# Kernel tuning notes

Measured on AMD Instinct MI355X. Metric: run time of the kernel, lower is better.

Reference implementation:

```python
import jax, jax.numpy as jnp
import numpy as np

B, L, D = 4096, 200, 32
NUM_USERS, NUM_GOODS, NUM_CATS = 49023, 143534, 4815
ATT_H1, ATT_H2 = 80, 40
MLP_H1, MLP_H2 = 200, 80
NEG_INF = jnp.float32(-2**32 + 1)


def prelu(x, a):
    return jnp.where(x >= 0, x, a * x)


def setup_inputs() -> dict:
    key = jax.random.key(0)
    ks = jax.random.split(key, 24)
    g = lambda k, shape, fan_in: jax.random.normal(k, shape, jnp.float32) * (1.0 / np.sqrt(fan_in))
    return {
        "uid": jax.random.randint(ks[0], (B,), 0, NUM_USERS, jnp.int32),
        "gid": jax.random.randint(ks[1], (B,), 0, NUM_GOODS, jnp.int32),
        "cid": jax.random.randint(ks[2], (B,), 0, NUM_CATS, jnp.int32),
        "gid_his": jax.random.randint(ks[3], (B, L), 0, NUM_GOODS, jnp.int32),
        "cid_his": jax.random.randint(ks[4], (B, L), 0, NUM_CATS, jnp.int32),
        "masks": jax.random.randint(ks[5], (B, L), 0, 2, jnp.int32),
        # frozen embedding tables
        "user_emb": jax.random.normal(ks[6], (NUM_USERS, D), jnp.float32),
        "good_emb": jax.random.normal(ks[7], (NUM_GOODS, D), jnp.float32),
        "cat_emb": jax.random.normal(ks[8], (NUM_CATS, D), jnp.float32),
        # attention MLP: 8D -> 80 -> 40 -> 1, sigmoid activations
        "att_w1": g(ks[9], (ATT_H1, 8 * D), 8 * D), "att_b1": jnp.zeros((ATT_H1,), jnp.float32),
        "att_w2": g(ks[10], (ATT_H2, ATT_H1), ATT_H1), "att_b2": jnp.zeros((ATT_H2,), jnp.float32),
        "att_w3": g(ks[11], (1, ATT_H2), ATT_H2), "att_b3": jnp.zeros((1,), jnp.float32),
        # final MLP: 9D -> 200 -> 80 -> 2, PReLU activations
        "mlp_w1": g(ks[12], (MLP_H1, 9 * D), 9 * D), "mlp_b1": jnp.zeros((MLP_H1,), jnp.float32),
        "mlp_w2": g(ks[13], (MLP_H2, MLP_H1), MLP_H1), "mlp_b2": jnp.zeros((MLP_H2,), jnp.float32),
        "mlp_w3": g(ks[14], (2, MLP_H2), MLP_H2), "mlp_b3": jnp.zeros((2,), jnp.float32),
        "a1": jnp.full((MLP_H1,), 0.25, jnp.float32),
        "a2": jnp.full((MLP_H2,), 0.25, jnp.float32),
    }


def reference(uid, gid, cid, gid_his, cid_his, masks,
              user_emb, good_emb, cat_emb,
              att_w1, att_b1, att_w2, att_b2, att_w3, att_b3,
              mlp_w1, mlp_b1, mlp_w2, mlp_b2, mlp_w3, mlp_b3, a1, a2):
    user = user_emb[uid]                                              # (B, D)
    query = jnp.concatenate([good_emb[gid], cat_emb[cid]], -1)        # (B, 2D)
    beh = jnp.concatenate([good_emb[gid_his], cat_emb[cid_his]], -1)  # (B, L, 2D)

    # attention: concat(query, behavior, diff, product) -> tiny MLP -> masked softmax pool
    q = jnp.broadcast_to(query[:, None, :], beh.shape)                # (B, L, 2D)
    s = jnp.concatenate([q, beh, q - beh, q * beh], -1)               # (B, L, 8D)
    s = jax.nn.sigmoid(jnp.einsum('blk,hk->blh', s, att_w1) + att_b1)
    s = jax.nn.sigmoid(jnp.einsum('blh,gh->blg', s, att_w2) + att_b2)
    s = jnp.einsum('blg,og->blo', s, att_w3) + att_b3                 # (B, L, 1)
    s = jnp.where(masks[..., None].astype(bool), s, NEG_INF)
    w = jax.nn.softmax(s, axis=1)
    att = jnp.sum(w * beh, axis=1)                                    # (B, 2D)

    ubs = beh.sum(axis=1)                                             # (B, 2D)
    x = jnp.concatenate([user, query, ubs, ubs * query, att], -1)     # (B, 9D)
    x = prelu(x @ mlp_w1.T + mlp_b1, a1)
    x = prelu(x @ mlp_w2.T + mlp_b2, a2)
    return x @ mlp_w3.T + mlp_b3                                      # (B, 2)
```

## Files before the change

kernel.cpp:

```cpp
#include <hip/hip_runtime.h>
#include <math.h>

typedef unsigned short u16;
typedef unsigned int u32;
typedef __attribute__((ext_vector_type(8))) short short8;
typedef __attribute__((ext_vector_type(8))) float f32x8;
typedef __attribute__((ext_vector_type(4))) float f32x4;
typedef __attribute__((ext_vector_type(2))) unsigned int uint2v;

#define NEG_BIG   (-4294967296.0f)
#define NEG_INF_F (-__builtin_inff())

#define WS_S    0
#define WS_W1T  5120
#define WS_W2T  62720
#define WS_W3T  78720
#define WS_W3P  78880
#define WS_WF1F 78928
#define WS_WF2F 84048
#define WS_XF   86352

__device__ __forceinline__ u32 f2bf2(float lo, float hi) {
    u32 r;
    asm("v_cvt_pk_bf16_f32 %0, %1, %2" : "=v"(r) : "v"(lo), "v"(hi));
    return r;
}
__device__ __forceinline__ u16 f2bf(float f) {
    u32 r;
    asm("v_cvt_pk_bf16_f32 %0, %1, %1" : "=v"(r) : "v"(f));
    return (u16)r;
}
__device__ __forceinline__ float bf2f(u16 h) {
    union { u32 u; float f; } v; v.u = ((u32)h) << 16;
    return v.f;
}
__device__ __forceinline__ float fsigmoid(float x) {
    float e, r;
    float t = x * -1.44269504088896f;
    asm("v_exp_f32 %0, %1" : "=v"(e) : "v"(t));
    float d = 1.0f + e;
    asm("v_rcp_f32 %0, %1" : "=v"(r) : "v"(d));
    return r;
}
__device__ __forceinline__ short8 mulqf(short8 a, f32x8 qf) {
    union { u32 w[4]; short8 s; } r;
    #pragma unroll
    for (int j = 0; j < 4; ++j) {
        float p0 = bf2f((u16)a[2*j])   * qf[2*j];
        float p1 = bf2f((u16)a[2*j+1]) * qf[2*j+1];
        r.w[j] = f2bf2(p0, p1);
    }
    return r.s;
}
__device__ __forceinline__ f32x4 mfma16(short8 a, short8 b, f32x4 c) {
    return __builtin_amdgcn_mfma_f32_16x16x32_bf16(a, b, c, 0, 0, 0);
}

__global__ __launch_bounds__(256) void prep_kernel(
    const float* __restrict__ att_w1,
    const float* __restrict__ att_w2,
    const float* __restrict__ att_w3,
    const float* __restrict__ mlp_w1,
    const float* __restrict__ mlp_w2,
    const float* __restrict__ mlp_w3,
    float* __restrict__ ws)
{
    int idx = blockIdx.x * 256 + threadIdx.x;
    if (idx < 5120) {
        int h = idx >> 6, j = idx & 63;
        ws[WS_S + idx] = att_w1[h*256 + j] + att_w1[h*256 + 128 + j];
    } else if (idx < 62720) {
        int r = idx - 5120;
        int k = r / 200, t = r - k*200;
        ws[WS_W1T + r] = mlp_w1[t*288 + k];
    } else if (idx < 78720) {
        int r = idx - 62720;
        int k = r / 80, g = r - k*80;
        ws[WS_W2T + r] = mlp_w2[g*200 + k];
    } else if (idx < 78880) {
        int r = idx - 78720;
        int k = r >> 1, o = r & 1;
        ws[WS_W3T + r] = mlp_w3[o*80 + k];
    } else if (idx < 78928) {
        int g = idx - 78880;
        ws[WS_W3P + g] = (g < 40) ? att_w3[g] : 0.0f;
    } else if (idx < 89168) {
        int e  = idx - 78928;
        int nt = e >> 11;
        int ks = (e >> 9) & 3;
        int ln = (e >> 3) & 63;
        int j  = e & 7;
        int n = nt*16 + (ln & 15);
        int k = ks*32 + (ln >> 4)*8 + j;
        float val = (k < 64)
            ? (att_w1[n*256 + 64 + k] - att_w1[n*256 + 128 + k])
            : att_w1[n*256 + 192 + (k - 64)];
        ((u16*)(ws + WS_WF1F))[e] = f2bf(val);
    } else if (idx < 93776) {
        int e  = idx - 89168;
        int nt = e / 1536;
        int ks = (e / 512) % 3;
        int ln = (e >> 3) & 63;
        int j  = e & 7;
        int n = nt*16 + (ln & 15);
        int k = ks*32 + (ln >> 4)*8 + j;
        float val = (n < 40 && k < 80) ? att_w2[n*80 + k] : 0.0f;
        ((u16*)(ws + WS_WF2F))[e] = f2bf(val);
    }
}

__global__ __launch_bounds__(256) void din_kernel(
    const int* __restrict__ uid, const int* __restrict__ gid, const int* __restrict__ cid,
    const int* __restrict__ gid_his, const int* __restrict__ cid_his, const int* __restrict__ masks,
    const float* __restrict__ user_emb, const float* __restrict__ good_emb, const float* __restrict__ cat_emb,
    const float* __restrict__ att_b1, const float* __restrict__ att_b2, const float* __restrict__ att_b3,
    const float* __restrict__ ws, float* __restrict__ Xg)
{
    __shared__ u16 Xc[200*64];
    __shared__ u16 scr[4*1664];
    __shared__ float q_sh[64];
    __shared__ float c0_sh[80];
    __shared__ float sp_sh[256];
    __shared__ float scal_sh[2];

    float* redA  = (float*)scr;
    float* redU  = redA + 512;

    const int b    = blockIdx.x;
    const int tid  = threadIdx.x;
    const int lane = tid & 63;
    const int wv   = tid >> 6;
    const int lrow = lane & 15;
    const int lgrp = lane >> 4;

    const int* gh = gid_his + b*200;
    const int* ch = cid_his + b*200;

    short8 wf1r[20];
    short8 wf2r[9];
    float  w3v[10];
    {
        const short8* WF1 = (const short8*)(ws + WS_WF1F);
        const short8* WF2 = (const short8*)(ws + WS_WF2F);
        #pragma unroll
        for (int i = 0; i < 20; ++i) wf1r[i] = WF1[i*64 + lane];
        #pragma unroll
        for (int i = 0; i < 9; ++i)  wf2r[i] = WF2[i*64 + lane];
        #pragma unroll
        for (int i = 0; i < 10; ++i) w3v[i] = ws[WS_W3P + lgrp + 4*i];
    }

    #pragma unroll
    for (int it = 0; it < 12; ++it) {
        int idx = it*256 + tid;
        int l = idx >> 4, c = idx & 15;
        const float* src = (c < 8)
            ? (good_emb + (size_t)gh[l]*32 + (c & 7)*4)
            : (cat_emb  + (size_t)ch[l]*32 + (c & 7)*4);
        float4 v = *(const float4*)src;
        uint2v pk;
        pk[0] = f2bf2(v.x, v.y);
        pk[1] = f2bf2(v.z, v.w);
        int byteoff = l*128 + ((((c >> 1) ^ (l & 7)) << 4)) + ((c & 1) << 3);
        *((uint2v*)((char*)Xc + byteoff)) = pk;
    }
    if (tid < 128) {
        int idx = 3072 + tid;
        int l = idx >> 4, c = idx & 15;
        const float* src = (c < 8)
            ? (good_emb + (size_t)gh[l]*32 + (c & 7)*4)
            : (cat_emb  + (size_t)ch[l]*32 + (c & 7)*4);
        float4 v = *(const float4*)src;
        uint2v pk;
        pk[0] = f2bf2(v.x, v.y);
        pk[1] = f2bf2(v.z, v.w);
        int byteoff = l*128 + ((((c >> 1) ^ (l & 7)) << 4)) + ((c & 1) << 3);
        *((uint2v*)((char*)Xc + byteoff)) = pk;
    }
    if (tid < 64) {
        q_sh[tid] = (tid < 32) ? good_emb[(size_t)gid[b]*32 + tid]
                               : cat_emb[(size_t)cid[b]*32 + (tid - 32)];
    }
    if (tid >= 200 && tid < 256) sp_sh[tid] = NEG_INF_F;
    __syncthreads();

    if (tid < 80) {
        const float4* Sw = (const float4*)(ws + WS_S + tid*64);
        const float4* q4 = (const float4*)q_sh;
        float u0 = 0.f, u1 = 0.f;
        #pragma unroll
        for (int j = 0; j < 16; j += 2) {
            float4 w0 = Sw[j],   qv0 = q4[j];
            float4 w1 = Sw[j+1], qv1 = q4[j+1];
            u0 += w0.x*qv0.x + w0.y*qv0.y + w0.z*qv0.z + w0.w*qv0.w;
            u1 += w1.x*qv1.x + w1.y*qv1.y + w1.z*qv1.z + w1.w*qv1.w;
        }
        c0_sh[tid] = att_b1[tid] + u0 + u1;
    }
    __syncthreads();

    f32x8 qf0, qf1;
    #pragma unroll
    for (int j = 0; j < 8; ++j) {
        qf0[j] = q_sh[lgrp*8 + j];
        qf1[j] = q_sh[32 + lgrp*8 + j];
    }
    float c0v[5];
    #pragma unroll
    for (int nt = 0; nt < 5; ++nt) c0v[nt] = c0_sh[nt*16 + lrow];
    float b2v[3];
    #pragma unroll
    for (int nt = 0; nt < 3; ++nt) {
        int col = nt*16 + lrow;
        b2v[nt] = (col < 40) ? att_b2[col] : 0.0f;
    }
    const float bias3 = att_b3[0];

    u16*   scr_w = scr + wv*1664;
    float* scr_f = (float*)scr_w;

    {
        uint2v z; z[0] = 0u; z[1] = 0u;
        *((uint2v*)(scr_w + lrow*104 + 80 + lgrp*4)) = z;
    }

    for (int t = wv; t < 13; t += 4) {
        const int m0 = (t == 12) ? 184 : (t << 4);
        const int m  = m0 + lrow;

        short8 A0, A1;
        {
            int sl0 = (0 + lgrp) ^ (m & 7);
            int sl1 = (4 + lgrp) ^ (m & 7);
            A0 = *(const short8*)((const char*)Xc + m*128 + (sl0 << 4));
            A1 = *(const short8*)((const char*)Xc + m*128 + (sl1 << 4));
        }
        short8 A2 = mulqf(A0, qf0);
        short8 A3 = mulqf(A1, qf1);

        #pragma unroll
        for (int nt = 0; nt < 5; ++nt) {
            f32x4 acc = {0.f, 0.f, 0.f, 0.f};
            acc = mfma16(A0, wf1r[nt*4 + 0], acc);
            acc = mfma16(A1, wf1r[nt*4 + 1], acc);
            acc = mfma16(A2, wf1r[nt*4 + 2], acc);
            acc = mfma16(A3, wf1r[nt*4 + 3], acc);
            #pragma unroll
            for (int r = 0; r < 4; ++r) {
                float s1v = fsigmoid(acc[r] + c0v[nt]);
                scr_w[(lgrp*4 + r)*104 + nt*16 + lrow] = f2bf(s1v);
            }
        }

        short8 B0 = *(const short8*)(scr_w + lrow*104 +  0 + lgrp*8);
        short8 B1 = *(const short8*)(scr_w + lrow*104 + 32 + lgrp*8);
        short8 B2 = *(const short8*)(scr_w + lrow*104 + 64 + lgrp*8);
        #pragma unroll
        for (int nt = 0; nt < 3; ++nt) {
            f32x4 acc = {0.f, 0.f, 0.f, 0.f};
            acc = mfma16(B0, wf2r[nt*3 + 0], acc);
            acc = mfma16(B1, wf2r[nt*3 + 1], acc);
            acc = mfma16(B2, wf2r[nt*3 + 2], acc);
            #pragma unroll
            for (int r = 0; r < 4; ++r) {
                float s2v = fsigmoid(acc[r] + b2v[nt]);
                scr_f[(lgrp*4 + r)*52 + nt*16 + lrow] = s2v;
            }
        }

        float v3 = 0.f;
        #pragma unroll
        for (int i = 0; i < 10; ++i) {
            v3 += scr_f[lrow*52 + lgrp + 4*i] * w3v[i];
        }
        v3 += __shfl_xor(v3, 16);
        v3 += __shfl_xor(v3, 32);
        if (lane < 16) {
            int mm = m0 + lane;
            float sval = v3 + bias3;
            int mk = masks[b*200 + mm];
            sp_sh[mm] = mk ? sval : NEG_BIG;
        }
    }
    __syncthreads();

    if (tid < 64) {
        float mv = fmaxf(fmaxf(sp_sh[tid], sp_sh[tid+64]), fmaxf(sp_sh[tid+128], sp_sh[tid+192]));
        #pragma unroll
        for (int off = 32; off > 0; off >>= 1) mv = fmaxf(mv, __shfl_down(mv, off));
        if (tid == 0) scal_sh[0] = mv;
    }
    __syncthreads();
    {
        float mx = scal_sh[0];
        float sm = sp_sh[tid];
        float ev = (tid < 200) ? __expf(sm - mx) : 0.0f;
        sp_sh[tid] = ev;
    }
    __syncthreads();
    if (tid < 64) {
        float s = (sp_sh[tid] + sp_sh[tid+64]) + (sp_sh[tid+128] + sp_sh[tid+192]);
        #pragma unroll
        for (int off = 32; off > 0; off >>= 1) s += __shfl_down(s, off);
        if (tid == 0) scal_sh[1] = s;
    }
    __syncthreads();

    {
        int j2 = tid & 31;
        int qq = tid >> 5;
        int slot = j2 >> 2;
        int inb  = (j2 & 3) << 2;
        float a0 = 0.f, a1 = 0.f, u0 = 0.f, u1 = 0.f;
        #pragma unroll 5
        for (int mm = qq*25; mm < qq*25 + 25; ++mm) {
            u32 pr = *(const u32*)((const char*)Xc + mm*128 + (((slot ^ (mm & 7)) << 4)) + inb);
            float b0 = bf2f((u16)pr);
            float b1_ = bf2f((u16)(pr >> 16));
            float w = sp_sh[mm];
            a0 += w*b0; a1 += w*b1_;
            u0 += b0;   u1 += b1_;
        }
        redA[qq*64 + 2*j2]     = a0;
        redA[qq*64 + 2*j2 + 1] = a1;
        redU[qq*64 + 2*j2]     = u0;
        redU[qq*64 + 2*j2 + 1] = u1;
    }
    __syncthreads();

    float inv = 1.0f / scal_sh[1];
    if (tid < 64) {
        float att = 0.f, ub = 0.f;
        #pragma unroll
        for (int qq = 0; qq < 8; ++qq) {
            att += redA[qq*64 + tid];
            ub  += redU[qq*64 + tid];
        }
        att *= inv;
        float qv = q_sh[tid];
        float* xr = Xg + (size_t)b*288;
        xr[32  + tid] = qv;
        xr[96  + tid] = ub;
        xr[160 + tid] = ub * qv;
        xr[224 + tid] = att;
    }
    if (tid >= 64 && tid < 96) {
        Xg[(size_t)b*288 + (tid - 64)] = user_emb[(size_t)uid[b]*32 + (tid - 64)];
    }
}

__global__ __launch_bounds__(256) void mlp_kernel(
    const float* __restrict__ ws,
    const float* __restrict__ mlp_b1, const float* __restrict__ mlp_b2, const float* __restrict__ mlp_b3,
    const float* __restrict__ pa1, const float* __restrict__ pa2,
    float* __restrict__ out)
{
    __shared__ float h1_sh[8*204];
    __shared__ float h2_sh[8*81];

    const int tid = threadIdx.x;
    const int r0  = blockIdx.x * 8;
    const float* Xg  = ws + WS_XF;
    const float* w1T = ws + WS_W1T;
    const float* w2T = ws + WS_W2T;
    const float* w3T = ws + WS_W3T;

    {
        int n = (tid < 200) ? tid : 199;
        float bias = mlp_b1[n];
        float acc[8];
        #pragma unroll
        for (int r = 0; r < 8; ++r) acc[r] = bias;
        for (int k = 0; k < 288; k += 4) {
            float w0 = w1T[(k+0)*200 + n];
            float w1 = w1T[(k+1)*200 + n];
            float w2 = w1T[(k+2)*200 + n];
            float w3 = w1T[(k+3)*200 + n];
            #pragma unroll
            for (int r = 0; r < 8; ++r) {
                const float4 xv = *(const float4*)(Xg + (size_t)(r0 + r)*288 + k);
                acc[r] += xv.x*w0 + xv.y*w1 + xv.z*w2 + xv.w*w3;
            }
        }
        if (tid < 200) {
            float a = pa1[n];
            #pragma unroll
            for (int r = 0; r < 8; ++r) {
                float v = acc[r];
                h1_sh[r*204 + n] = (v >= 0.f) ? v : a*v;
            }
        }
    }
    __syncthreads();

    if (tid < 160) {
        int g  = (tid < 80) ? tid : tid - 80;
        int rh = (tid < 80) ? 0 : 4;
        float bias = mlp_b2[g];
        float acc[4];
        #pragma unroll
        for (int r = 0; r < 4; ++r) acc[r] = bias;
        for (int k = 0; k < 200; k += 4) {
            float w0 = w2T[(k+0)*80 + g];
            float w1 = w2T[(k+1)*80 + g];
            float w2 = w2T[(k+2)*80 + g];
            float w3 = w2T[(k+3)*80 + g];
            #pragma unroll
            for (int r = 0; r < 4; ++r) {
                const float4 xv = *(const float4*)(&h1_sh[(rh + r)*204 + k]);
                acc[r] += xv.x*w0 + xv.y*w1 + xv.z*w2 + xv.w*w3;
            }
        }
        float a = pa2[g];
        #pragma unroll
        for (int r = 0; r < 4; ++r) {
            float v = acc[r];
            h2_sh[(rh + r)*81 + g] = (v >= 0.f) ? v : a*v;
        }
    }
    __syncthreads();

    if (tid < 16) {
        int r = tid >> 1, o = tid & 1;
        float acc = mlp_b3[o];
        #pragma unroll 8
        for (int k = 0; k < 80; ++k) acc += h2_sh[r*81 + k] * w3T[k*2 + o];
        out[(size_t)(r0 + r)*2 + o] = acc;
    }
}

extern "C" void kernel_launch(void* const* d_in, const int* in_sizes, int n_in,
                              void* d_out, int out_size, void* d_ws, size_t ws_size,
                              hipStream_t stream) {
    const int*   uid      = (const int*)d_in[0];
    const int*   gid      = (const int*)d_in[1];
    const int*   cid      = (const int*)d_in[2];
    const int*   gid_his  = (const int*)d_in[3];
    const int*   cid_his  = (const int*)d_in[4];
    const int*   masks    = (const int*)d_in[5];
    const float* user_emb = (const float*)d_in[6];
    const float* good_emb = (const float*)d_in[7];
    const float* cat_emb  = (const float*)d_in[8];
    const float* att_w1   = (const float*)d_in[9];
    const float* att_b1   = (const float*)d_in[10];
    const float* att_w2   = (const float*)d_in[11];
    const float* att_b2   = (const float*)d_in[12];
    const float* att_w3   = (const float*)d_in[13];
    const float* att_b3   = (const float*)d_in[14];
    const float* mlp_w1   = (const float*)d_in[15];
    const float* mlp_b1   = (const float*)d_in[16];
    const float* mlp_w2   = (const float*)d_in[17];
    const float* mlp_b2   = (const float*)d_in[18];
    const float* mlp_w3   = (const float*)d_in[19];
    const float* mlp_b3   = (const float*)d_in[20];
    const float* pa1      = (const float*)d_in[21];
    const float* pa2      = (const float*)d_in[22];
    float* ws   = (float*)d_ws;
    float* outp = (float*)d_out;

    hipLaunchKernelGGL(prep_kernel, dim3(367), dim3(256), 0, stream,
                       att_w1, att_w2, att_w3, mlp_w1, mlp_w2, mlp_w3, ws);
    hipLaunchKernelGGL(din_kernel, dim3(4096), dim3(256), 0, stream,
                       uid, gid, cid, gid_his, cid_his, masks,
                       user_emb, good_emb, cat_emb,
                       att_b1, att_b2, att_b3,
                       ws, ws + WS_XF);
    hipLaunchKernelGGL(mlp_kernel, dim3(512), dim3(256), 0, stream,
                       ws, mlp_b1, mlp_b2, mlp_b3, pa1, pa2, outp);
}
```

Before: 150.5 us.

## Move att layer-2 weights to LDS, fuse layer-3 dot via shuffles, raise occupancy

Layer-2 attention MFMA weight fragments now live in shared memory instead of per-thread registers. Layer-3 now multiplies sigmoid outputs directly in the accumulator layout and reduces them with lane shuffles, which removes the fp32 scratch round trip through LDS. Launch bounds request three blocks per SM, so the compiler must cap register use. In exchange the kernel adds LDS reads of B operands on every tile and uses more shared memory, which may itself cap occupancy.

```diff
diff --git a/kernel.cpp b/kernel.cpp
--- a/kernel.cpp
+++ b/kernel.cpp
@@ -109,7 +109,7 @@
     }
 }
 
-__global__ __launch_bounds__(256) void din_kernel(
+__global__ __launch_bounds__(256, 3) void din_kernel(
     const int* __restrict__ uid, const int* __restrict__ gid, const int* __restrict__ cid,
     const int* __restrict__ gid_his, const int* __restrict__ cid_his, const int* __restrict__ masks,
     const float* __restrict__ user_emb, const float* __restrict__ good_emb, const float* __restrict__ cat_emb,
@@ -118,6 +118,7 @@
 {
     __shared__ u16 Xc[200*64];
     __shared__ u16 scr[4*1664];
+    __shared__ u16 wf2_sh[9*512];
     __shared__ float q_sh[64];
     __shared__ float c0_sh[80];
     __shared__ float sp_sh[256];
@@ -137,17 +138,16 @@
     const int* ch = cid_his + b*200;
 
     short8 wf1r[20];
-    short8 wf2r[9];
-    float  w3v[10];
     {
         const short8* WF1 = (const short8*)(ws + WS_WF1F);
-        const short8* WF2 = (const short8*)(ws + WS_WF2F);
         #pragma unroll
         for (int i = 0; i < 20; ++i) wf1r[i] = WF1[i*64 + lane];
-        #pragma unroll
-        for (int i = 0; i < 9; ++i)  wf2r[i] = WF2[i*64 + lane];
-        #pragma unroll
-        for (int i = 0; i < 10; ++i) w3v[i] = ws[WS_W3P + lgrp + 4*i];
+    }
+    {
+        const u32* src = (const u32*)(ws + WS_WF2F);
+        u32* dst = (u32*)wf2_sh;
+        #pragma unroll
+        for (int i = 0; i < 9; ++i) dst[i*256 + tid] = src[i*256 + tid];
     }
 
     #pragma unroll
@@ -208,16 +208,16 @@
     float c0v[5];
     #pragma unroll
     for (int nt = 0; nt < 5; ++nt) c0v[nt] = c0_sh[nt*16 + lrow];
-    float b2v[3];
+    float b2v[3], w3c[3];
     #pragma unroll
     for (int nt = 0; nt < 3; ++nt) {
         int col = nt*16 + lrow;
         b2v[nt] = (col < 40) ? att_b2[col] : 0.0f;
+        w3c[nt] = ws[WS_W3P + col];
     }
     const float bias3 = att_b3[0];
 
-    u16*   scr_w = scr + wv*1664;
-    float* scr_f = (float*)scr_w;
+    u16* scr_w = scr + wv*1664;
 
     {
         uint2v z; z[0] = 0u; z[1] = 0u;
@@ -255,31 +255,35 @@
         short8 B0 = *(const short8*)(scr_w + lrow*104 +  0 + lgrp*8);
         short8 B1 = *(const short8*)(scr_w + lrow*104 + 32 + lgrp*8);
         short8 B2 = *(const short8*)(scr_w + lrow*104 + 64 + lgrp*8);
+        f32x4 acc2[3];
         #pragma unroll
         for (int nt = 0; nt < 3; ++nt) {
             f32x4 acc = {0.f, 0.f, 0.f, 0.f};
-            acc = mfma16(B0, wf2r[nt*3 + 0], acc);
-            acc = mfma16(B1, wf2r[nt*3 + 1], acc);
-            acc = mfma16(B2, wf2r[nt*3 + 2], acc);
+            acc = mfma16(B0, *(const short8*)(wf2_sh + ((nt*3 + 0)*64 + lane)*8), acc);
+            acc = mfma16(B1, *(const short8*)(wf2_sh + ((nt*3 + 1)*64 + lane)*8), acc);
+            acc = mfma16(B2, *(const short8*)(wf2_sh + ((nt*3 + 2)*64 + lane)*8), acc);
+            acc2[nt] = acc;
+        }
+
+        float v3p[4];
+        #pragma unroll
+        for (int r = 0; r < 4; ++r) {
+            float p = fsigmoid(acc2[0][r] + b2v[0]) * w3c[0]
+                    + fsigmoid(acc2[1][r] + b2v[1]) * w3c[1]
+                    + fsigmoid(acc2[2][r] + b2v[2]) * w3c[2];
+            p += __shfl_xor(p, 1);
+            p += __shfl_xor(p, 2);
+            p += __shfl_xor(p, 4);
+            p += __shfl_xor(p, 8);
+            v3p[r] = p;
+        }
+        if (lrow == 0) {
             #pragma unroll
             for (int r = 0; r < 4; ++r) {
-                float s2v = fsigmoid(acc[r] + b2v[nt]);
-                scr_f[(lgrp*4 + r)*52 + nt*16 + lrow] = s2v;
+                int mm = m0 + lgrp*4 + r;
+                int mk = masks[b*200 + mm];
+                sp_sh[mm] = mk ? (v3p[r] + bias3) : NEG_BIG;
             }
-        }
-
-        float v3 = 0.f;
-        #pragma unroll
-        for (int i = 0; i < 10; ++i) {
-            v3 += scr_f[lrow*52 + lgrp + 4*i] * w3v[i];
-        }
-        v3 += __shfl_xor(v3, 16);
-        v3 += __shfl_xor(v3, 32);
-        if (lane < 16) {
-            int mm = m0 + lane;
-            float sval = v3 + bias3;
-            int mk = masks[b*200 + mm];
-            sp_sh[mm] = mk ? sval : NEG_BIG;
         }
     }
     __syncthreads();
```

New measurement: 130.4 us (median of 3 runs). 13.4% less time.
